# Kernel optimization log

Hardware: AMD Instinct MI355X
Metric: run time of the kernel (lower is better)

## Reference

```python
import jax, jax.numpy as jnp
import numpy as np

BS, D, M = 64, 256, 512


def setup_inputs() -> dict:
    key = jax.random.key(0)
    ks = jax.random.split(key, 6)
    # Small scales keep the 10-step RLS recurrence numerically stable.
    A_start = 0.05 * jax.random.normal(ks[0], (BS, D, D), dtype=jnp.float32)
    Y1 = 0.05 * jax.random.normal(ks[1], (BS, D, M), dtype=jnp.float32)
    Y2 = 0.05 * jax.random.normal(ks[2], (BS, D, M), dtype=jnp.float32)
    y1 = 0.05 * jax.random.normal(ks[3], (BS, D, 1), dtype=jnp.float32)
    y2 = 0.05 * jax.random.normal(ks[4], (BS, D, 1), dtype=jnp.float32)
    eye = jnp.broadcast_to(jnp.eye(D, dtype=jnp.float32), (BS, D, D))
    P_inv_start = 1e-3 * eye + 1e-4 * jax.random.normal(ks[5], (BS, D, D), dtype=jnp.float32)
    return {"A_start": A_start, "Y1": Y1, "Y2": Y2, "y1": y1, "y2": y2,
            "P_inv_start": P_inv_start, "h": 2, "m_prox": 10}


def _t(x):
    return jnp.swapaxes(x, 1, 2)


def reference(A_start, Y1, Y2, y1, y2, P_inv_start, h, m_prox):
    """Faithful jax version of DelayedDMD.update.

    The torch code recomputes `A_t + P_inv @ (Y1 @ (Y2^T - Y1^T @ A_t))` twice
    per step; here it is computed once (same math, fused).
    """
    Y1t, Y2t, y1t, y2t = _t(Y1), _t(Y2), _t(y1), _t(y2)
    denom = 1.0 + y1t @ P_inv_start @ y1          # (bs, 1, 1)
    Piy1 = P_inv_start @ y1                       # (bs, d, 1)

    def step(A_t, _):
        # batch recursive-least-squares prox iteration
        M_ = A_t + P_inv_start @ (Y1 @ (Y2t - Y1t @ A_t))   # (bs, d, d)
        A_new = M_ + y1 @ (y2t - y1t @ M_) / denom
        return A_new, None

    A_final_t, _ = jax.lax.scan(step, _t(A_start), None, length=m_prox)
    P_inv_new = P_inv_start - Piy1 @ (y1t @ P_inv_start) / denom
    return _t(A_final_t), P_inv_new
```

## Files before the change

### kernel.cpp

```cpp
#include <hip/hip_runtime.h>
#include <hip/hip_bf16.h>
#include <stdint.h>


#define BSZ 64
#define DD 256
#define MM 512

typedef __attribute__((ext_vector_type(8))) short short8;
typedef __attribute__((ext_vector_type(4))) float f32x4;

__device__ __forceinline__ unsigned short f2b(float f) {
    unsigned int u = __float_as_uint(f);
    unsigned int r = (u + 0x7fffu + ((u >> 16) & 1u)) >> 16;
    return (unsigned short)r;
}
__device__ __forceinline__ float b2f(unsigned short s) {
    return __uint_as_float(((unsigned int)s) << 16);
}
__device__ __forceinline__ void gll16(const void* g, void* l) {
    __builtin_amdgcn_global_load_lds(
        (const __attribute__((address_space(1))) unsigned int*)g,
        (__attribute__((address_space(3))) unsigned int*)l, 16, 0, 0);
}


__global__ __launch_bounds__(256)
void prep1(const float* __restrict__ P, const float* __restrict__ y1g,
           unsigned short* __restrict__ Pb, float* __restrict__ vec,
           float* __restrict__ qpart)
{
    const int blk = blockIdx.x, t = threadIdx.x;
    const int b = blk >> 3, rs = (blk & 7) * 32;
    const long base = (long)b * DD * DD;
    const int wv = t >> 6, ln = t & 63;
    __shared__ float sy1[DD];
    __shared__ float qsh[4][DD];
    sy1[t] = y1g[b * DD + t];
    __syncthreads();
    const int col4 = ln * 4;
    const float4 yv = *(const float4*)(sy1 + col4);
    float4 pr[8];
#pragma unroll
    for (int i = 0; i < 8; ++i) {
        const int row = rs + i * 4 + wv;
        pr[i] = *(const float4*)(P + base + (long)row * DD + col4);
    }
    float ql0 = 0.f, ql1 = 0.f, ql2 = 0.f, ql3 = 0.f;
#pragma unroll
    for (int i = 0; i < 8; ++i) {
        const int row = rs + i * 4 + wv;
        const long o = base + (long)row * DD + col4;
        const float4 p = pr[i];
        ushort4 u;
        u.x = f2b(p.x); u.y = f2b(p.y); u.z = f2b(p.z); u.w = f2b(p.w);
        *(ushort4*)(Pb + o) = u;
        const float yr = sy1[row];
        ql0 += yr * p.x; ql1 += yr * p.y; ql2 += yr * p.z; ql3 += yr * p.w;
        float s = p.x * yv.x + p.y * yv.y + p.z * yv.z + p.w * yv.w;
#pragma unroll
        for (int off = 32; off; off >>= 1) s += __shfl_down(s, off, 64);
        if (ln == 0) vec[(long)b * 768 + row] = s;
    }
    *(float4*)(qsh[wv] + col4) = make_float4(ql0, ql1, ql2, ql3);
    __syncthreads();
    qpart[((long)blk) * DD + t] = qsh[0][t] + qsh[1][t] + qsh[2][t] + qsh[3][t];
}

__global__ __launch_bounds__(256)
void prep2e(const float* __restrict__ Y1, const float* __restrict__ Y2,
            const float* __restrict__ y1g, const float* __restrict__ qpart,
            unsigned short* __restrict__ G1b, unsigned short* __restrict__ G21b,
            float* __restrict__ vec)
{
    const int blk = blockIdx.x, t = threadIdx.x;
    if (blk >= 512) {
        const int b = blk - 512;
        float* vb = vec + (long)b * 768;
        const float* qp = qpart + (long)b * 8 * DD;
        float qv = 0.f;
#pragma unroll
        for (int c = 0; c < 8; ++c) qv += qp[c * DD + t];
        vb[256 + t] = qv;
        __shared__ float red[256];
        red[t] = vb[t] * y1g[b * DD + t];
        __syncthreads();
        for (int s = 128; s; s >>= 1) { if (t < s) red[t] += red[t + s]; __syncthreads(); }
        if (t == 0) vb[512] = 1.0f / (1.0f + red[0]);
        return;
    }
    __shared__ __align__(16) unsigned short S[2][8192];
    const int b = (blk & 7) + 8 * ((blk >> 3) & 7), tile = blk >> 6;
    const int i0 = (tile & 3) * 64, j0 = (tile >> 2) * 128;
    const float* A1 = Y1 + (long)b * DD * MM + (long)i0 * MM;
    const float* A2 = Y2 + (long)b * DD * MM + (long)i0 * MM;
    const float* By = Y1 + (long)b * DD * MM + (long)j0 * MM;
    const int wv = t >> 6, ln = t & 63;
    const int lr = ln & 15, qd = ln >> 4;
    const int wr = wv >> 1, wc = wv & 1;
    f32x4 acc1[2][4] = {}, acc2[2][4] = {};
    float4 fr[8];

#define P2LOAD(kc)                                                            \
    do {                                                                      \
        _Pragma("unroll")                                                     \
        for (int i = 0; i < 2; ++i) {                                         \
            const int s = i * 256 + t, row = s >> 3, c4 = s & 7;              \
            const long go = (long)row * MM + (kc) * 32 + c4 * 4;              \
            fr[i]     = *(const float4*)(A1 + go);                            \
            fr[2 + i] = *(const float4*)(A2 + go);                            \
        }                                                                     \
        _Pragma("unroll")                                                     \
        for (int i = 0; i < 4; ++i) {                                         \
            const int s = i * 256 + t, row = s >> 3, c4 = s & 7;              \
            const long go = (long)row * MM + (kc) * 32 + c4 * 4;              \
            fr[4 + i] = *(const float4*)(By + go);                            \
        }                                                                     \
    } while (0)

    P2LOAD(0);
    for (int kc = 0; kc < 16; ++kc) {
        const int u = kc & 1;
#pragma unroll
        for (int i = 0; i < 2; ++i) {
            const int s = i * 256 + t, row = s >> 3, c4 = s & 7;
            const int line = row >> 1;
            const int g8 = (((row & 1) << 2) + (c4 >> 1)) ^ (line & 7);
            const int off = line * 128 + (g8 << 4) + ((c4 & 1) << 3);
            ushort4 ua, ub;
            ua.x = f2b(fr[i].x); ua.y = f2b(fr[i].y);
            ua.z = f2b(fr[i].z); ua.w = f2b(fr[i].w);
            ub.x = f2b(fr[2 + i].x); ub.y = f2b(fr[2 + i].y);
            ub.z = f2b(fr[2 + i].z); ub.w = f2b(fr[2 + i].w);
            *(ushort4*)((char*)S[u] + off) = ua;
            *(ushort4*)((char*)S[u] + 4096 + off) = ub;
        }
#pragma unroll
        for (int i = 0; i < 4; ++i) {
            const int s = i * 256 + t, row = s >> 3, c4 = s & 7;
            const int line = row >> 1;
            const int g8 = (((row & 1) << 2) + (c4 >> 1)) ^ (line & 7);
            const int off = line * 128 + (g8 << 4) + ((c4 & 1) << 3);
            ushort4 uc;
            uc.x = f2b(fr[4 + i].x); uc.y = f2b(fr[4 + i].y);
            uc.z = f2b(fr[4 + i].z); uc.w = f2b(fr[4 + i].w);
            *(ushort4*)((char*)S[u] + 8192 + off) = uc;
        }
        __syncthreads();
        if (kc < 15) { P2LOAD(kc + 1); }
        short8 a1[2], a2[2], bfr[4];
#pragma unroll
        for (int mt = 0; mt < 2; ++mt) {
            const int row = wr * 32 + mt * 16 + lr;
            const int line = row >> 1;
            const int off = line * 128 + (((((row & 1) << 2) + qd) ^ (line & 7)) << 4);
            a1[mt] = *(const short8*)((const char*)S[u] + off);
            a2[mt] = *(const short8*)((const char*)S[u] + 4096 + off);
        }
#pragma unroll
        for (int nt = 0; nt < 4; ++nt) {
            const int row = wc * 64 + nt * 16 + lr;
            const int line = row >> 1;
            const int off = line * 128 + (((((row & 1) << 2) + qd) ^ (line & 7)) << 4);
            bfr[nt] = *(const short8*)((const char*)S[u] + 8192 + off);
        }
#pragma unroll
        for (int mt = 0; mt < 2; ++mt)
#pragma unroll
            for (int nt = 0; nt < 4; ++nt) {
                acc1[mt][nt] = __builtin_amdgcn_mfma_f32_16x16x32_bf16(
                    a1[mt], bfr[nt], acc1[mt][nt], 0, 0, 0);
                acc2[mt][nt] = __builtin_amdgcn_mfma_f32_16x16x32_bf16(
                    a2[mt], bfr[nt], acc2[mt][nt], 0, 0, 0);
            }
    }
#undef P2LOAD
    unsigned short* O1 = G1b  + (long)b * DD * DD;
    unsigned short* O2 = G21b + (long)b * DD * DD;
#pragma unroll
    for (int mt = 0; mt < 2; ++mt)
#pragma unroll
        for (int nt = 0; nt < 4; ++nt) {
            const int gr0 = i0 + wr * 32 + mt * 16 + qd * 4;
            const int gc  = j0 + wc * 64 + nt * 16 + lr;
#pragma unroll
            for (int r = 0; r < 4; ++r) {
                O1[(long)(gr0 + r) * DD + gc] = f2b(acc1[mt][nt][r]);
                O2[(long)(gr0 + r) * DD + gc] = f2b(acc2[mt][nt][r]);
            }
        }
}

__global__ __launch_bounds__(256)
void gemmEV(const unsigned short* __restrict__ Pb, const unsigned short* __restrict__ G1b,
            const unsigned short* __restrict__ G21b,
            const float* __restrict__ y1g, const float* __restrict__ y2g,
            const float* __restrict__ vec,
            unsigned short* __restrict__ Enb, unsigned short* __restrict__ Vpb)
{
    __shared__ __align__(16) unsigned short S[2][2][128 * 64];
    __shared__ float qs[DD], s1[DD], s2[DD];
    const int blk = blockIdx.x, t = threadIdx.x;
    const int b = (blk & 7) + 8 * (blk >> 6);
    const int rem = (blk >> 3) & 7, sel = rem >> 2, quad = rem & 3;
    const int i0 = (quad >> 1) * 128, j0 = (quad & 1) * 128;
    const char* Ab = (const char*)((sel ? G21b : Pb) + (long)b * DD * DD + (long)i0 * DD);
    const char* Bb = (const char*)((sel ? Pb : G1b) + (long)b * DD * DD + (long)j0 * DD);
    unsigned short* Ob = (sel ? Vpb : Enb) + (long)b * DD * DD;
    const float* vb = vec + (long)b * 768;
    const int wv = t >> 6, ln = t & 63;
    const int lr = ln & 15, qd = ln >> 4;
    const int mh = (wv >> 1) * 64, nh = (wv & 1) * 64;
    const int srow = t >> 3;
    const int sc = (t & 7) * 16;

    qs[t] = vb[256 + t];
    s1[t] = y1g[b * DD + t];
    s2[t] = y2g[b * DD + t];

    f32x4 acc[4][4] = {};
    float dot[4] = {0.f, 0.f, 0.f, 0.f};

#define GEVSTAGE(u, kc)                                                           \
    _Pragma("unroll")                                                             \
    for (int i = 0; i < 4; ++i) {                                                 \
        const int row = i * 32 + srow;                                            \
        const int gco = (kc) * 128 + (sc ^ ((row & 7) << 4));                     \
        const int lo = row * 128 + sc;                                            \
        gll16(Ab + (long)row * 512 + gco, (char*)S[u][0] + lo);                   \
        gll16(Bb + (long)row * 512 + gco, (char*)S[u][1] + lo);                   \
    }

    GEVSTAGE(0, 0);
    for (int kc = 0; kc < 4; ++kc) {
        __syncthreads();
        if (kc < 3) { GEVSTAGE((kc + 1) & 1, kc + 1); }
        const unsigned short (*Su)[128 * 64] = S[kc & 1];
#pragma unroll
        for (int kc2 = 0; kc2 < 2; ++kc2) {
            const int kb = kc2 * 64 + qd * 16;
            short8 af[4], bfr[4];
#pragma unroll
            for (int mt = 0; mt < 4; ++mt) {
                const int row = mh + mt * 16 + lr;
                af[mt] = *(const short8*)((const char*)Su[0] + row * 128 +
                                          (kb ^ ((row & 7) << 4)));
            }
#pragma unroll
            for (int nt = 0; nt < 4; ++nt) {
                const int row = nh + nt * 16 + lr;
                bfr[nt] = *(const short8*)((const char*)Su[1] + row * 128 +
                                           (kb ^ ((row & 7) << 4)));
            }
            const int kel = kc * 64 + kc2 * 32 + qd * 8;
            const float4 qa = *(const float4*)(qs + kel);
            const float4 qb = *(const float4*)(qs + kel + 4);
            const float qf[8] = {qa.x, qa.y, qa.z, qa.w, qb.x, qb.y, qb.z, qb.w};
            if (!sel) {
#pragma unroll
                for (int nt = 0; nt < 4; ++nt)
#pragma unroll
                    for (int j = 0; j < 8; ++j)
                        dot[nt] += b2f((unsigned short)bfr[nt][j]) * qf[j];
            } else {
#pragma unroll
                for (int mt = 0; mt < 4; ++mt)
#pragma unroll
                    for (int j = 0; j < 8; ++j)
                        dot[mt] += b2f((unsigned short)af[mt][j]) * qf[j];
            }
#pragma unroll
            for (int mt = 0; mt < 4; ++mt)
#pragma unroll
                for (int nt = 0; nt < 4; ++nt)
                    acc[mt][nt] = __builtin_amdgcn_mfma_f32_16x16x32_bf16(
                        af[mt], bfr[nt], acc[mt][nt], 0, 0, 0);
        }
    }
#undef GEVSTAGE
#pragma unroll
    for (int i = 0; i < 4; ++i) {
        dot[i] += __shfl_xor(dot[i], 16, 64);
        dot[i] += __shfl_xor(dot[i], 32, 64);
    }
    const float kk = vb[512];
#pragma unroll
    for (int mt = 0; mt < 4; ++mt) {
#pragma unroll
        for (int nt = 0; nt < 4; ++nt) {
            const int gr0 = i0 + mh + mt * 16 + qd * 4;
            const int gc  = j0 + nh + nt * 16 + lr;
            if (!sel) {
                const float cw = s1[gc] - dot[nt];
#pragma unroll
                for (int r = 0; r < 4; ++r) {
                    const float rv = kk * s1[gr0 + r];
                    Ob[(long)(gr0 + r) * DD + gc] = f2b(-(acc[mt][nt][r] + rv * cw));
                }
            } else {
                const float cv = s1[gc];
#pragma unroll
                for (int r = 0; r < 4; ++r) {
                    const float uv = __shfl(dot[mt], qd * 4 + r, 64);
                    const float rv = kk * (s2[gr0 + r] - uv);
                    Ob[(long)(gr0 + r) * DD + gc] = f2b(acc[mt][nt][r] + rv * cv);
                }
            }
        }
    }
}

__global__ __launch_bounds__(256, 2)
void iterk(const float* __restrict__ A_start, const unsigned short* __restrict__ Enb,
           const unsigned short* __restrict__ Vpb,
           const unsigned short* __restrict__ Pb, const float* __restrict__ vec,
           float* __restrict__ out1, float* __restrict__ out2)
{
    const int blk = blockIdx.x, t = threadIdx.x;
    if (blk >= 512) {
        const int c = blk - 512, b = (c & 7) + 8 * (c >> 5), rs = ((c >> 3) & 3) * 64;
        const long base = (long)b * DD * DD;
        const float* vb = vec + (long)b * 768;
        const float kk = vb[512];
#pragma unroll 4
        for (int i = 0; i < 16; ++i) {
            const int idx = rs * DD + (i * 256 + t) * 4;
            const int row = idx >> 8, col = idx & 255;
            const float kPi = kk * vb[row];
            const ushort4 pu = *(const ushort4*)(Pb + base + idx);
            const float4 q = *(const float4*)(vb + 256 + col);
            float4 rr;
            rr.x = b2f(pu.x) - kPi * q.x; rr.y = b2f(pu.y) - kPi * q.y;
            rr.z = b2f(pu.z) - kPi * q.z; rr.w = b2f(pu.w) - kPi * q.w;
            *(float4*)(out2 + base + idx) = rr;
        }
        return;
    }
    __shared__ __align__(16) unsigned short Xsh[32 * 256];
    const int b = (blk & 7) + 8 * (blk >> 6), r0 = ((blk >> 3) & 7) * 32;
    const long base = (long)b * DD * DD;
    const float* Ab = A_start + base;
    const unsigned short* Eb = Enb + base;
    const unsigned short* Vb = Vpb + base;
    float* Ob = out1 + base;
    const int wv = t >> 6, ln = t & 63;
    const int lr = ln & 15, qd = ln >> 4;
    const int ib = wv * 64;

    f32x4 acc[4][2], vv[4][2];
    short8 ef[4][8];

#pragma unroll
    for (int it = 0; it < 4; ++it)
#pragma unroll
        for (int jt = 0; jt < 2; ++jt) {
            const long o = (long)(r0 + jt * 16 + lr) * DD + ib + it * 16 + qd * 4;
            acc[it][jt] = *(const f32x4*)(Ab + o);
            const ushort4 vu = *(const ushort4*)(Vb + o);
            vv[it][jt][0] = b2f(vu.x); vv[it][jt][1] = b2f(vu.y);
            vv[it][jt][2] = b2f(vu.z); vv[it][jt][3] = b2f(vu.w);
        }
#pragma unroll
    for (int it = 0; it < 4; ++it) {
        const long ro = (long)(ib + it * 16 + lr) * DD;
#pragma unroll
        for (int kc = 0; kc < 8; ++kc)
            ef[it][kc] = *(const short8*)(Eb + ro + kc * 32 + qd * 8);
    }

    const int gpart = wv * 8 + (qd >> 1), off8 = (qd & 1) * 8;

#pragma unroll 1
    for (int s = 0; s < 10; ++s) {
#pragma unroll
        for (int it = 0; it < 4; ++it)
#pragma unroll
            for (int jt = 0; jt < 2; ++jt) {
                const int j = jt * 16 + lr;
                const int g = (gpart + it * 2) ^ ((j & 7) << 1);
                const unsigned int p0 = (unsigned int)f2b(acc[it][jt][0]) |
                                        ((unsigned int)f2b(acc[it][jt][1]) << 16);
                const unsigned int p1 = (unsigned int)f2b(acc[it][jt][2]) |
                                        ((unsigned int)f2b(acc[it][jt][3]) << 16);
                *(uint2*)((char*)Xsh + j * 512 + g * 16 + off8) = make_uint2(p0, p1);
                acc[it][jt] += vv[it][jt];
            }
        __syncthreads();
#pragma unroll
        for (int kc = 0; kc < 8; ++kc) {
            short8 bf[2];
#pragma unroll
            for (int jt = 0; jt < 2; ++jt) {
                const int j = jt * 16 + lr;
                const int g = (kc * 4 + qd) ^ ((j & 7) << 1);
                bf[jt] = *(const short8*)((char*)Xsh + j * 512 + g * 16);
            }
#pragma unroll
            for (int it = 0; it < 4; ++it)
#pragma unroll
                for (int jt = 0; jt < 2; ++jt)
                    acc[it][jt] = __builtin_amdgcn_mfma_f32_16x16x32_bf16(
                        ef[it][kc], bf[jt], acc[it][jt], 0, 0, 0);
        }
        __syncthreads();
    }

#pragma unroll
    for (int it = 0; it < 4; ++it)
#pragma unroll
        for (int jt = 0; jt < 2; ++jt) {
            const long o = (long)(r0 + jt * 16 + lr) * DD + ib + it * 16 + qd * 4;
            *(f32x4*)(Ob + o) = acc[it][jt];
        }
}

extern "C" void kernel_launch(void* const* d_in, const int* in_sizes, int n_in,
                              void* d_out, int out_size, void* d_ws, size_t ws_size,
                              hipStream_t stream)
{
    const float* A_start = (const float*)d_in[0];
    const float* Y1      = (const float*)d_in[1];
    const float* Y2      = (const float*)d_in[2];
    const float* y1      = (const float*)d_in[3];
    const float* y2      = (const float*)d_in[4];
    const float* P       = (const float*)d_in[5];

    const long EL2 = (long)BSZ * DD * DD;

    float* out1 = (float*)d_out;
    float* out2 = out1 + EL2;

    char* w8 = (char*)d_ws;
    unsigned short* Pb    = (unsigned short*)(w8);
    unsigned short* G1b   = (unsigned short*)(w8 + 8388608);
    unsigned short* G21b  = (unsigned short*)(w8 + 16777216);
    unsigned short* Enb   = (unsigned short*)(w8 + 25165824);
    unsigned short* Vpb   = (unsigned short*)(w8 + 33554432);
    float*          vec   = (float*)(w8 + 41943040);
    float*          qpart = (float*)(w8 + 42139648);

    const dim3 blk(256);

    prep1<<<512, blk, 0, stream>>>(P, y1, Pb, vec, qpart);
    prep2e<<<576, blk, 0, stream>>>(Y1, Y2, y1, qpart, G1b, G21b, vec);
    gemmEV<<<512, blk, 0, stream>>>(Pb, G1b, G21b, y1, y2, vec, Enb, Vpb);
    iterk<<<768, blk, 0, stream>>>(A_start, Enb, Vpb, Pb, vec, out1, out2);
}
```

Measured before the change: 195.5 us.

## Merge prep kernels and fold P_inv update and scalar reductions into gemmEV

```diff
diff --git a/kernel.cpp b/kernel.cpp
--- a/kernel.cpp
+++ b/kernel.cpp
@@ -26,70 +26,52 @@
 
 
 __global__ __launch_bounds__(256)
-void prep1(const float* __restrict__ P, const float* __restrict__ y1g,
-           unsigned short* __restrict__ Pb, float* __restrict__ vec,
-           float* __restrict__ qpart)
+void prep12(const float* __restrict__ P, const float* __restrict__ y1g,
+            const float* __restrict__ Y1, const float* __restrict__ Y2,
+            unsigned short* __restrict__ Pb,
+            unsigned short* __restrict__ G1b, unsigned short* __restrict__ G21b,
+            float* __restrict__ vec, float* __restrict__ qpart)
 {
     const int blk = blockIdx.x, t = threadIdx.x;
-    const int b = blk >> 3, rs = (blk & 7) * 32;
-    const long base = (long)b * DD * DD;
-    const int wv = t >> 6, ln = t & 63;
+    __shared__ __align__(16) unsigned short S[2][8192];
     __shared__ float sy1[DD];
     __shared__ float qsh[4][DD];
-    sy1[t] = y1g[b * DD + t];
-    __syncthreads();
-    const int col4 = ln * 4;
-    const float4 yv = *(const float4*)(sy1 + col4);
-    float4 pr[8];
-#pragma unroll
-    for (int i = 0; i < 8; ++i) {
-        const int row = rs + i * 4 + wv;
-        pr[i] = *(const float4*)(P + base + (long)row * DD + col4);
-    }
-    float ql0 = 0.f, ql1 = 0.f, ql2 = 0.f, ql3 = 0.f;
-#pragma unroll
-    for (int i = 0; i < 8; ++i) {
-        const int row = rs + i * 4 + wv;
-        const long o = base + (long)row * DD + col4;
-        const float4 p = pr[i];
-        ushort4 u;
-        u.x = f2b(p.x); u.y = f2b(p.y); u.z = f2b(p.z); u.w = f2b(p.w);
-        *(ushort4*)(Pb + o) = u;
-        const float yr = sy1[row];
-        ql0 += yr * p.x; ql1 += yr * p.y; ql2 += yr * p.z; ql3 += yr * p.w;
-        float s = p.x * yv.x + p.y * yv.y + p.z * yv.z + p.w * yv.w;
-#pragma unroll
-        for (int off = 32; off; off >>= 1) s += __shfl_down(s, off, 64);
-        if (ln == 0) vec[(long)b * 768 + row] = s;
-    }
-    *(float4*)(qsh[wv] + col4) = make_float4(ql0, ql1, ql2, ql3);
-    __syncthreads();
-    qpart[((long)blk) * DD + t] = qsh[0][t] + qsh[1][t] + qsh[2][t] + qsh[3][t];
-}
-
-__global__ __launch_bounds__(256)
-void prep2e(const float* __restrict__ Y1, const float* __restrict__ Y2,
-            const float* __restrict__ y1g, const float* __restrict__ qpart,
-            unsigned short* __restrict__ G1b, unsigned short* __restrict__ G21b,
-            float* __restrict__ vec)
-{
-    const int blk = blockIdx.x, t = threadIdx.x;
     if (blk >= 512) {
-        const int b = blk - 512;
-        float* vb = vec + (long)b * 768;
-        const float* qp = qpart + (long)b * 8 * DD;
-        float qv = 0.f;
-#pragma unroll
-        for (int c = 0; c < 8; ++c) qv += qp[c * DD + t];
-        vb[256 + t] = qv;
-        __shared__ float red[256];
-        red[t] = vb[t] * y1g[b * DD + t];
-        __syncthreads();
-        for (int s = 128; s; s >>= 1) { if (t < s) red[t] += red[t + s]; __syncthreads(); }
-        if (t == 0) vb[512] = 1.0f / (1.0f + red[0]);
+        const int c = blk - 512;
+        const int b = c >> 3, rs = (c & 7) * 32;
+        const long base = (long)b * DD * DD;
+        const int wv = t >> 6, ln = t & 63;
+        sy1[t] = y1g[b * DD + t];
+        __syncthreads();
+        const int col4 = ln * 4;
+        const float4 yv = *(const float4*)(sy1 + col4);
+        float4 pr[8];
+#pragma unroll
+        for (int i = 0; i < 8; ++i) {
+            const int row = rs + i * 4 + wv;
+            pr[i] = *(const float4*)(P + base + (long)row * DD + col4);
+        }
+        float ql0 = 0.f, ql1 = 0.f, ql2 = 0.f, ql3 = 0.f;
+#pragma unroll
+        for (int i = 0; i < 8; ++i) {
+            const int row = rs + i * 4 + wv;
+            const long o = base + (long)row * DD + col4;
+            const float4 p = pr[i];
+            ushort4 u;
+            u.x = f2b(p.x); u.y = f2b(p.y); u.z = f2b(p.z); u.w = f2b(p.w);
+            *(ushort4*)(Pb + o) = u;
+            const float yr = sy1[row];
+            ql0 += yr * p.x; ql1 += yr * p.y; ql2 += yr * p.z; ql3 += yr * p.w;
+            float s = p.x * yv.x + p.y * yv.y + p.z * yv.z + p.w * yv.w;
+#pragma unroll
+            for (int off = 32; off; off >>= 1) s += __shfl_down(s, off, 64);
+            if (ln == 0) vec[(long)b * 768 + row] = s;
+        }
+        *(float4*)(qsh[wv] + col4) = make_float4(ql0, ql1, ql2, ql3);
+        __syncthreads();
+        qpart[((long)c) * DD + t] = qsh[0][t] + qsh[1][t] + qsh[2][t] + qsh[3][t];
         return;
     }
-    __shared__ __align__(16) unsigned short S[2][8192];
     const int b = (blk & 7) + 8 * ((blk >> 3) & 7), tile = blk >> 6;
     const int i0 = (tile & 3) * 64, j0 = (tile >> 2) * 128;
     const float* A1 = Y1 + (long)b * DD * MM + (long)i0 * MM;
@@ -192,14 +174,15 @@
 }
 
 __global__ __launch_bounds__(256)
-void gemmEV(const unsigned short* __restrict__ Pb, const unsigned short* __restrict__ G1b,
-            const unsigned short* __restrict__ G21b,
-            const float* __restrict__ y1g, const float* __restrict__ y2g,
-            const float* __restrict__ vec,
-            unsigned short* __restrict__ Enb, unsigned short* __restrict__ Vpb)
+void gemmEVq(const unsigned short* __restrict__ Pb, const unsigned short* __restrict__ G1b,
+             const unsigned short* __restrict__ G21b,
+             const float* __restrict__ y1g, const float* __restrict__ y2g,
+             const float* __restrict__ vec, const float* __restrict__ qpart,
+             unsigned short* __restrict__ Enb, unsigned short* __restrict__ Vpb,
+             float* __restrict__ out2)
 {
     __shared__ __align__(16) unsigned short S[2][2][128 * 64];
-    __shared__ float qs[DD], s1[DD], s2[DD];
+    __shared__ float qs[DD], s1[DD], s2[DD], pv[DD], red[DD];
     const int blk = blockIdx.x, t = threadIdx.x;
     const int b = (blk & 7) + 8 * (blk >> 6);
     const int rem = (blk >> 3) & 7, sel = rem >> 2, quad = rem & 3;
@@ -207,19 +190,11 @@
     const char* Ab = (const char*)((sel ? G21b : Pb) + (long)b * DD * DD + (long)i0 * DD);
     const char* Bb = (const char*)((sel ? Pb : G1b) + (long)b * DD * DD + (long)j0 * DD);
     unsigned short* Ob = (sel ? Vpb : Enb) + (long)b * DD * DD;
-    const float* vb = vec + (long)b * 768;
     const int wv = t >> 6, ln = t & 63;
     const int lr = ln & 15, qd = ln >> 4;
     const int mh = (wv >> 1) * 64, nh = (wv & 1) * 64;
     const int srow = t >> 3;
     const int sc = (t & 7) * 16;
-
-    qs[t] = vb[256 + t];
-    s1[t] = y1g[b * DD + t];
-    s2[t] = y2g[b * DD + t];
-
-    f32x4 acc[4][4] = {};
-    float dot[4] = {0.f, 0.f, 0.f, 0.f};
 
 #define GEVSTAGE(u, kc)                                                           \
     _Pragma("unroll")                                                             \
@@ -232,6 +207,24 @@
     }
 
     GEVSTAGE(0, 0);
+    {
+        const float* qp = qpart + (long)b * 8 * DD;
+        float qv = 0.f;
+#pragma unroll
+        for (int c = 0; c < 8; ++c) qv += qp[c * DD + t];
+        qs[t] = qv;
+        s1[t] = y1g[b * DD + t];
+        s2[t] = y2g[b * DD + t];
+        pv[t] = vec[(long)b * 768 + t];
+        red[t] = pv[t] * s1[t];
+        __syncthreads();
+        for (int s = 128; s; s >>= 1) { if (t < s) red[t] += red[t + s]; __syncthreads(); }
+    }
+    const float kk = 1.0f / (1.0f + red[0]);
+
+    f32x4 acc[4][4] = {};
+    float dot[4] = {0.f, 0.f, 0.f, 0.f};
+
     for (int kc = 0; kc < 4; ++kc) {
         __syncthreads();
         if (kc < 3) { GEVSTAGE((kc + 1) & 1, kc + 1); }
@@ -283,7 +276,6 @@
         dot[i] += __shfl_xor(dot[i], 16, 64);
         dot[i] += __shfl_xor(dot[i], 32, 64);
     }
-    const float kk = vb[512];
 #pragma unroll
     for (int mt = 0; mt < 4; ++mt) {
 #pragma unroll
@@ -308,34 +300,30 @@
             }
         }
     }
+    {
+        const long base = (long)b * DD * DD;
+        const int rs = rem * 32;
+#pragma unroll
+        for (int i = 0; i < 8; ++i) {
+            const int idx = rs * DD + (i * 256 + t) * 4;
+            const int row = idx >> 8, col = idx & 255;
+            const float kPi = kk * pv[row];
+            const ushort4 pu = *(const ushort4*)(Pb + base + idx);
+            float4 rr;
+            rr.x = b2f(pu.x) - kPi * qs[col];
+            rr.y = b2f(pu.y) - kPi * qs[col + 1];
+            rr.z = b2f(pu.z) - kPi * qs[col + 2];
+            rr.w = b2f(pu.w) - kPi * qs[col + 3];
+            *(float4*)(out2 + base + idx) = rr;
+        }
+    }
 }
 
 __global__ __launch_bounds__(256, 2)
 void iterk(const float* __restrict__ A_start, const unsigned short* __restrict__ Enb,
-           const unsigned short* __restrict__ Vpb,
-           const unsigned short* __restrict__ Pb, const float* __restrict__ vec,
-           float* __restrict__ out1, float* __restrict__ out2)
+           const unsigned short* __restrict__ Vpb, float* __restrict__ out1)
 {
     const int blk = blockIdx.x, t = threadIdx.x;
-    if (blk >= 512) {
-        const int c = blk - 512, b = (c & 7) + 8 * (c >> 5), rs = ((c >> 3) & 3) * 64;
-        const long base = (long)b * DD * DD;
-        const float* vb = vec + (long)b * 768;
-        const float kk = vb[512];
-#pragma unroll 4
-        for (int i = 0; i < 16; ++i) {
-            const int idx = rs * DD + (i * 256 + t) * 4;
-            const int row = idx >> 8, col = idx & 255;
-            const float kPi = kk * vb[row];
-            const ushort4 pu = *(const ushort4*)(Pb + base + idx);
-            const float4 q = *(const float4*)(vb + 256 + col);
-            float4 rr;
-            rr.x = b2f(pu.x) - kPi * q.x; rr.y = b2f(pu.y) - kPi * q.y;
-            rr.z = b2f(pu.z) - kPi * q.z; rr.w = b2f(pu.w) - kPi * q.w;
-            *(float4*)(out2 + base + idx) = rr;
-        }
-        return;
-    }
     __shared__ __align__(16) unsigned short Xsh[32 * 256];
     const int b = (blk & 7) + 8 * (blk >> 6), r0 = ((blk >> 3) & 7) * 32;
     const long base = (long)b * DD * DD;
@@ -441,8 +429,8 @@
 
     const dim3 blk(256);
 
-    prep1<<<512, blk, 0, stream>>>(P, y1, Pb, vec, qpart);
-    prep2e<<<576, blk, 0, stream>>>(Y1, Y2, y1, qpart, G1b, G21b, vec);
-    gemmEV<<<512, blk, 0, stream>>>(Pb, G1b, G21b, y1, y2, vec, Enb, Vpb);
-    iterk<<<768, blk, 0, stream>>>(A_start, Enb, Vpb, Pb, vec, out1, out2);
-}
+    prep12<<<1024, blk, 0, stream>>>(P, y1, Y1, Y2, Pb, G1b, G21b, vec, qpart);
+    gemmEVq<<<512, blk, 0, stream>>>(Pb, G1b, G21b, y1, y2, vec, qpart,
+                                     Enb, Vpb, out2);
+    iterk<<<512, blk, 0, stream>>>(A_start, Enb, Vpb, out1);
+}
```

Result: no change. 195.6 us (+0.0%).
